# Kernel optimization log

Hardware: AMD Instinct MI355X
Metric: run time of the kernel (lower is better)

The kernel has to match this reference:

```python
import jax, jax.numpy as jnp
import numpy as np

N, D, E, L = 50000, 128, 800000, 3
BN_EPS = 1e-5


def _bn(h, mean, var, gamma, beta):
    # eval-mode BatchNorm1d with running statistics
    return (h - mean) * jax.lax.rsqrt(var + BN_EPS) * gamma + beta


def setup_inputs() -> dict:
    key = jax.random.key(0)
    ks = jax.random.split(key, 16)
    x = jax.random.normal(ks[0], (N, D), dtype=jnp.float32)
    edge_index = jax.random.randint(ks[1], (2, E), 0, N, dtype=jnp.int32)
    s = 1.0 / np.sqrt(D)
    W1 = jax.random.uniform(ks[2], (L, D, 2 * D), jnp.float32, -s, s)
    b1 = jax.random.uniform(ks[3], (L, 2 * D), jnp.float32, -s, s)
    g1 = jnp.ones((L, 2 * D), jnp.float32)
    be1 = jnp.zeros((L, 2 * D), jnp.float32)
    m1 = jax.random.normal(ks[4], (L, 2 * D), jnp.float32) * 0.1
    v1 = jax.random.uniform(ks[5], (L, 2 * D), jnp.float32, 0.5, 1.5)
    s2 = 1.0 / np.sqrt(2 * D)
    W2 = jax.random.uniform(ks[6], (L, 2 * D, D), jnp.float32, -s2, s2)
    b2 = jax.random.uniform(ks[7], (L, D), jnp.float32, -s2, s2)
    eps = jnp.zeros((L,), jnp.float32)  # train_eps=True, init 0
    go = jnp.ones((L - 1, D), jnp.float32)
    bo = jnp.zeros((L - 1, D), jnp.float32)
    mo = jax.random.normal(ks[8], (L - 1, D), jnp.float32) * 0.1
    vo = jax.random.uniform(ks[9], (L - 1, D), jnp.float32, 0.5, 1.5)
    return {"x": x, "edge_index": edge_index, "W1": W1, "b1": b1, "g1": g1,
            "be1": be1, "m1": m1, "v1": v1, "W2": W2, "b2": b2, "eps": eps,
            "go": go, "bo": bo, "mo": mo, "vo": vo}


def reference(x, edge_index, W1, b1, g1, be1, m1, v1, W2, b2, eps, go, bo, mo, vo):
    src, dst = edge_index[0], edge_index[1]
    n = x.shape[0]
    h = x
    for i in range(L):
        # GINConv: (1+eps)*x_i + sum_{j in N(i)} x_j, then MLP
        agg = jax.ops.segment_sum(h[src], dst, num_segments=n)  # [N, D]
        z = (1.0 + eps[i]) * h + agg
        z = jax.nn.relu(_bn(z @ W1[i] + b1[i], m1[i], v1[i], g1[i], be1[i]))
        z = z @ W2[i] + b2[i]
        if i < L - 1:
            z = jax.nn.relu(_bn(z, mo[i], vo[i], go[i], bo[i]))
            # dropout: identity in eval mode
        h = z
    return jax.nn.log_softmax(h, axis=-1)
```

## Files before the change

### kernel.cpp

```cpp
#include <hip/hip_runtime.h>
#include <hip/hip_bf16.h>

#define N_NODES 50000
#define DIM 128
#define E_EDGES 800000
#define L_LAYERS 3
#define MTILES 3125
#define MTPAD 3128
#define NBUCK 98
#define BCAP 9216
#define BSHIFT 9

typedef __attribute__((ext_vector_type(8))) short short8;
typedef __attribute__((ext_vector_type(4))) float f32x4;
typedef __attribute__((ext_vector_type(2))) _Float16 f16x2;
typedef __attribute__((ext_vector_type(4))) _Float16 f16x4;
typedef __attribute__((ext_vector_type(8))) _Float16 f16x8;

__global__ __launch_bounds__(256) void cvt16_kernel(const float4* __restrict__ in,
                                                    f16x4* __restrict__ out) {
    int i = blockIdx.x * 256 + threadIdx.x;
    float4 v = in[i];
    f16x4 o;
    o[0] = (_Float16)v.x; o[1] = (_Float16)v.y;
    o[2] = (_Float16)v.z; o[3] = (_Float16)v.w;
    out[i] = o;
}

__global__ __launch_bounds__(256) void trans_f16_kernel(
        const float* __restrict__ w1, const float* __restrict__ w2,
        _Float16* __restrict__ f1, _Float16* __restrict__ f2) {
    int idx = blockIdx.x * 256 + threadIdx.x;
    const int per = DIM * 2 * DIM;
    const int tot = L_LAYERS * per;
    const float* w;
    _Float16* f;
    int K, Nn, id;
    if (idx < tot) { w = w1; f = f1; K = DIM; Nn = 2 * DIM; id = idx; }
    else           { w = w2; f = f2; K = 2 * DIM; Nn = DIM; id = idx - tot; }
    int l = id / per;
    int r = id - l * per;
    int k = r / Nn;
    int n = r - k * Nn;
    int KS = K >> 5;
    int off = ((((n >> 4) * KS + (k >> 5)) * 4 + ((k >> 3) & 3)) * 16 + (n & 15)) * 8 + (k & 7);
    f[(size_t)l * per + off] = (_Float16)w[id];
}

__global__ __launch_bounds__(256) void prep_params_kernel(
        const float* __restrict__ b1, const float* __restrict__ g1,
        const float* __restrict__ be1, const float* __restrict__ m1,
        const float* __restrict__ v1, const float* __restrict__ b2,
        const float* __restrict__ go, const float* __restrict__ bo,
        const float* __restrict__ mo, const float* __restrict__ vo,
        float* __restrict__ scale1, float* __restrict__ shift1,
        float* __restrict__ scale2, float* __restrict__ shift2) {
    int idx = blockIdx.x * 256 + threadIdx.x;
    if (idx < L_LAYERS * 256) {
        float s = g1[idx] * rsqrtf(v1[idx] + 1e-5f);
        scale1[idx] = s;
        shift1[idx] = (b1[idx] - m1[idx]) * s + be1[idx];
    }
    int idx2 = idx - L_LAYERS * 256;
    if (idx2 >= 0 && idx2 < L_LAYERS * 128) {
        int l = idx2 >> 7;
        if (l < L_LAYERS - 1) {
            float s = go[idx2] * rsqrtf(vo[idx2] + 1e-5f);
            scale2[idx2] = s;
            shift2[idx2] = (b2[idx2] - mo[idx2]) * s + bo[idx2];
        } else {
            scale2[idx2] = 1.0f;
            shift2[idx2] = b2[idx2];
        }
    }
}


__global__ void initcur_kernel(int* __restrict__ gcur) {
    int t = threadIdx.x;
    if (t < NBUCK) gcur[t] = t * BCAP;
}

__global__ __launch_bounds__(256) void bin_kernel(const int* __restrict__ ei,
                                                  int* __restrict__ gcur,
                                                  unsigned int* __restrict__ brec) {
    __shared__ int cnt[NBUCK];
    __shared__ int off[NBUCK];
    __shared__ int gbase[NBUCK];
    __shared__ unsigned int rec[4096];
    const int t = threadIdx.x;
    const int start = blockIdx.x * 4096;
    for (int i = t; i < NBUCK; i += 256) cnt[i] = 0;
    __syncthreads();
    unsigned int myrec[16];
    unsigned int mypos[16];
    int nmine = 0;
    #pragma unroll
    for (int i = 0; i < 16; ++i) {
        int e = start + i * 256 + t;
        if (e < E_EDGES) {
            int src = ei[e];
            int dst = ei[E_EDGES + e];
            int b = dst >> BSHIFT;
            int idx = atomicAdd(&cnt[b], 1);
            myrec[i] = ((unsigned int)(dst & 511) << 16) | (unsigned int)src;
            mypos[i] = ((unsigned int)b << 16) | (unsigned int)idx;
            nmine = i + 1;
        }
    }
    __syncthreads();
    if (t == 0) {
        int s = 0;
        for (int b = 0; b < NBUCK; ++b) { off[b] = s; s += cnt[b]; }
    }
    __syncthreads();
    #pragma unroll
    for (int i = 0; i < 16; ++i) {
        if (i < nmine) {
            int b = mypos[i] >> 16;
            int idx = mypos[i] & 0xFFFF;
            rec[off[b] + idx] = myrec[i];
        }
    }
    __syncthreads();
    if (t < NBUCK && cnt[t] > 0) gbase[t] = atomicAdd(&gcur[t], cnt[t]);
    __syncthreads();
    const int wv = t >> 6, lane = t & 63;
    for (int b = wv; b < NBUCK; b += 4) {
        int c = cnt[b], o = off[b], g = gbase[b];
        for (int j = lane; j < c; j += 64)
            brec[g + j] = rec[o + j];
    }
}

__global__ void bscan_kernel(const int* __restrict__ gcur, int* __restrict__ colbase,
                             int* __restrict__ rowp) {
    if (threadIdx.x == 0) {
        int s = 0;
        for (int b = 0; b < NBUCK; ++b) {
            colbase[b] = s;
            s += gcur[b] - b * BCAP;
        }
        rowp[N_NODES] = E_EDGES;
    }
}

__global__ __launch_bounds__(256) void bsort_kernel(const unsigned int* __restrict__ brec,
                                                    const int* __restrict__ gcur,
                                                    const int* __restrict__ colbase,
                                                    int* __restrict__ rowp,
                                                    unsigned short* __restrict__ col) {
    __shared__ int ncnt[512];
    __shared__ int noff[512];
    __shared__ int wsum[4];
    __shared__ unsigned short srcbuf[BCAP];
    const int b = blockIdx.x;
    const int t = threadIdx.x;
    const int lane = t & 63;
    const int wv = t >> 6;
    const int cnt = gcur[b] - b * BCAP;
    const unsigned int* r = brec + (size_t)b * BCAP;
    for (int i = t; i < 512; i += 256) ncnt[i] = 0;
    __syncthreads();
    for (int j = t; j < cnt; j += 256)
        atomicAdd(&ncnt[r[j] >> 16], 1);
    __syncthreads();
    int a0 = ncnt[2 * t], a1 = ncnt[2 * t + 1];
    int pair = a0 + a1;
    int inc = pair;
    #pragma unroll
    for (int d = 1; d < 64; d <<= 1) {
        int u = __shfl_up(inc, d, 64);
        if (lane >= d) inc += u;
    }
    if (lane == 63) wsum[wv] = inc;
    __syncthreads();
    int wo = 0;
    if (wv > 0) wo = wsum[0];
    if (wv > 1) wo += wsum[1];
    if (wv > 2) wo += wsum[2];
    int excl = wo + inc - pair;
    noff[2 * t] = excl;
    noff[2 * t + 1] = excl + a0;
    __syncthreads();
    const int n0 = b << BSHIFT;
    const int cb = colbase[b];
    for (int i = t; i < 512; i += 256) {
        int node = n0 + i;
        if (node < N_NODES) rowp[node] = cb + noff[i];
    }
    for (int i = t; i < 512; i += 256) ncnt[i] = noff[i];
    __syncthreads();
    for (int j = t; j < cnt; j += 256) {
        unsigned int v = r[j];
        int pos = atomicAdd(&ncnt[v >> 16], 1);
        srcbuf[pos] = (unsigned short)(v & 0xFFFFu);
    }
    __syncthreads();
    unsigned short* cp = col + cb;
    for (int j = t; j < cnt; j += 256) cp[j] = srcbuf[j];
}

__global__ __launch_bounds__(256) void aggregate_kernel(
        const unsigned int* __restrict__ h16,
        const int* __restrict__ row, const unsigned short* __restrict__ col,
        const float* __restrict__ epsp,
        unsigned short* __restrict__ zf) {
    int wv = threadIdx.x >> 6;
    int lane = threadIdx.x & 63;
    int node = blockIdx.x * 4 + wv;
    size_t base = (size_t)node * 64;
    float s = 1.0f + epsp[0];
    f16x2 hv = __builtin_bit_cast(f16x2, h16[base + lane]);
    float ax = s * (float)hv[0], ay = s * (float)hv[1];
    int e = row[node], e1 = row[node + 1];
    for (; e + 8 <= e1; e += 8) {
        int c0 = col[e],     c1 = col[e + 1], c2 = col[e + 2], c3 = col[e + 3];
        int c4 = col[e + 4], c5 = col[e + 5], c6 = col[e + 6], c7 = col[e + 7];
        f16x2 v0 = __builtin_bit_cast(f16x2, h16[(size_t)c0 * 64 + lane]);
        f16x2 v1 = __builtin_bit_cast(f16x2, h16[(size_t)c1 * 64 + lane]);
        f16x2 v2 = __builtin_bit_cast(f16x2, h16[(size_t)c2 * 64 + lane]);
        f16x2 v3 = __builtin_bit_cast(f16x2, h16[(size_t)c3 * 64 + lane]);
        f16x2 v4 = __builtin_bit_cast(f16x2, h16[(size_t)c4 * 64 + lane]);
        f16x2 v5 = __builtin_bit_cast(f16x2, h16[(size_t)c5 * 64 + lane]);
        f16x2 v6 = __builtin_bit_cast(f16x2, h16[(size_t)c6 * 64 + lane]);
        f16x2 v7 = __builtin_bit_cast(f16x2, h16[(size_t)c7 * 64 + lane]);
        ax += (((float)v0[0] + (float)v1[0]) + ((float)v2[0] + (float)v3[0]))
            + (((float)v4[0] + (float)v5[0]) + ((float)v6[0] + (float)v7[0]));
        ay += (((float)v0[1] + (float)v1[1]) + ((float)v2[1] + (float)v3[1]))
            + (((float)v4[1] + (float)v5[1]) + ((float)v6[1] + (float)v7[1]));
    }
    for (; e < e1; ++e) {
        f16x2 v = __builtin_bit_cast(f16x2, h16[(size_t)col[e] * 64 + lane]);
        ax += (float)v[0];
        ay += (float)v[1];
    }
    unsigned short ux = __builtin_bit_cast(unsigned short, (_Float16)ax);
    unsigned short uy = __builtin_bit_cast(unsigned short, (_Float16)ay);
    int mt = node >> 4, r16 = node & 15;
    int ks = lane >> 4, quad = (lane >> 2) & 3, jb = (lane * 2) & 7;
    size_t zo = (((size_t)(mt * 4 + ks)) * 4 + quad) * 128 + r16 * 8 + jb;
    *(ushort2*)(zf + zo) = make_ushort2(ux, uy);
}

__global__ __launch_bounds__(256) void mlp_kernel(
        const _Float16* __restrict__ zf,
        const _Float16* __restrict__ w1f, const _Float16* __restrict__ w2f,
        const float* __restrict__ scale1, const float* __restrict__ shift1,
        const float* __restrict__ scale2, const float* __restrict__ shift2,
        int last,
        unsigned short* __restrict__ h16out, float* __restrict__ lsout) {
    __shared__ _Float16 wbuf[16384];
    __shared__ _Float16 tbuf[4][2176];
    const int tid = threadIdx.x;
    const int wave = tid >> 6;
    const int lane = tid & 63;
    const int quad = lane >> 4;
    const int l16 = lane & 15;
    const int mt = blockIdx.x * 4 + wave;
    const int R0 = mt * 16;

    f16x8 ah[4];
    #pragma unroll
    for (int ks = 0; ks < 4; ++ks)
        ah[ks] = *(const f16x8*)(zf + (((size_t)(mt * 4 + ks)) << 9) + lane * 8);

    f32x4 acc2[8] = {};
    #pragma unroll
    for (int c = 0; c < 2; ++c) {
        {
            const _Float16* g = w1f + c * 16384 + tid * 8;
            _Float16* l = wbuf + tid * 8;
            #pragma unroll
            for (int j = 0; j < 8; ++j)
                *(f16x8*)(l + j * 2048) = *(const f16x8*)(g + j * 2048);
        }
        __syncthreads();
        #pragma unroll
        for (int ntl = 0; ntl < 8; ++ntl) {
            f32x4 acc = {};
            #pragma unroll
            for (int ks = 0; ks < 4; ++ks) {
                f16x8 b = *(const f16x8*)&wbuf[(ntl * 4 + ks) * 512 + lane * 8];
                acc = __builtin_amdgcn_mfma_f32_16x16x32_f16(ah[ks], b, acc, 0, 0, 0);
            }
            int cg = (c * 8 + ntl) * 16 + l16;
            float sc = scale1[cg];
            float sh = shift1[cg];
            int plane = (cg >> 3) & 15;
            int basei = plane * 136 + (cg & 7);
            #pragma unroll
            for (int r = 0; r < 4; ++r) {
                float val = fmaxf(acc[r] * sc + sh, 0.0f);
                tbuf[wave][basei + (quad * 4 + r) * 8] = (_Float16)val;
            }
        }
        __syncthreads();
        {
            #pragma unroll
            for (int nt = 0; nt < 8; ++nt) {
                *(f16x8*)&wbuf[nt * 2048 + tid * 8] =
                    *(const f16x8*)(w2f + (((size_t)(nt * 8 + c * 4)) << 9) + tid * 8);
            }
        }
        __syncthreads();
        #pragma unroll
        for (int ks4 = 0; ks4 < 4; ++ks4) {
            int po = (ks4 * 4 + quad) * 136 + l16 * 8;
            f16x8 a2 = *(const f16x8*)&tbuf[wave][po];
            #pragma unroll
            for (int nt = 0; nt < 8; ++nt) {
                f16x8 b = *(const f16x8*)&wbuf[(nt * 4 + ks4) * 512 + lane * 8];
                acc2[nt] = __builtin_amdgcn_mfma_f32_16x16x32_f16(a2, b, acc2[nt], 0, 0, 0);
            }
        }
        __syncthreads();
    }

    #pragma unroll
    for (int nt = 0; nt < 8; ++nt) {
        int cg = nt * 16 + l16;
        float sc = scale2[cg];
        float sh = shift2[cg];
        #pragma unroll
        for (int r = 0; r < 4; ++r)
            acc2[nt][r] = acc2[nt][r] * sc + sh;
    }
    if (!last) {
        #pragma unroll
        for (int nt = 0; nt < 8; ++nt) {
            int cg = nt * 16 + l16;
            #pragma unroll
            for (int r = 0; r < 4; ++r) {
                int rg = R0 + quad * 4 + r;
                if (rg < N_NODES) {
                    float val = fmaxf(acc2[nt][r], 0.0f);
                    h16out[(size_t)rg * DIM + cg] =
                        __builtin_bit_cast(unsigned short, (_Float16)val);
                }
            }
        }
    } else {
        #pragma unroll
        for (int r = 0; r < 4; ++r) {
            float mx = acc2[0][r];
            #pragma unroll
            for (int nt = 1; nt < 8; ++nt) mx = fmaxf(mx, acc2[nt][r]);
            #pragma unroll
            for (int off = 1; off < 16; off <<= 1) mx = fmaxf(mx, __shfl_xor(mx, off, 64));
            float sum = 0.0f;
            #pragma unroll
            for (int nt = 0; nt < 8; ++nt) sum += expf(acc2[nt][r] - mx);
            #pragma unroll
            for (int off = 1; off < 16; off <<= 1) sum += __shfl_xor(sum, off, 64);
            float ls = mx + logf(sum);
            int rg = R0 + quad * 4 + r;
            if (rg < N_NODES) {
                #pragma unroll
                for (int nt = 0; nt < 8; ++nt)
                    lsout[(size_t)rg * DIM + nt * 16 + l16] = acc2[nt][r] - ls;
            }
        }
    }
}

extern "C" void kernel_launch(void* const* d_in, const int* in_sizes, int n_in,
                              void* d_out, int out_size, void* d_ws, size_t ws_size,
                              hipStream_t stream) {
    const float* x   = (const float*)d_in[0];
    const int*   ei  = (const int*)d_in[1];
    const float* W1  = (const float*)d_in[2];
    const float* b1  = (const float*)d_in[3];
    const float* g1  = (const float*)d_in[4];
    const float* be1 = (const float*)d_in[5];
    const float* m1  = (const float*)d_in[6];
    const float* v1  = (const float*)d_in[7];
    const float* W2  = (const float*)d_in[8];
    const float* b2  = (const float*)d_in[9];
    const float* eps = (const float*)d_in[10];
    const float* go  = (const float*)d_in[11];
    const float* bo  = (const float*)d_in[12];
    const float* mo  = (const float*)d_in[13];
    const float* vo  = (const float*)d_in[14];

    char* ws = (char*)d_ws;
    unsigned short* h16 = (unsigned short*)ws;  ws += (size_t)N_NODES * DIM * 2;
    unsigned short* zf = (unsigned short*)ws;   ws += (size_t)MTPAD * 2048 * 2;
    _Float16* w1f = (_Float16*)ws;              ws += (size_t)L_LAYERS * 32768 * 2;
    _Float16* w2f = (_Float16*)ws;              ws += (size_t)L_LAYERS * 32768 * 2;
    float* scale1 = (float*)ws; ws += (size_t)L_LAYERS * 256 * 4;
    float* shift1 = (float*)ws; ws += (size_t)L_LAYERS * 256 * 4;
    float* scale2 = (float*)ws; ws += (size_t)L_LAYERS * 128 * 4;
    float* shift2 = (float*)ws; ws += (size_t)L_LAYERS * 128 * 4;
    unsigned int* brec = (unsigned int*)ws; ws += (size_t)NBUCK * BCAP * 4;
    int* gcur    = (int*)ws; ws += 128 * 4;
    int* colbase = (int*)ws; ws += 128 * 4;
    int* rowp    = (int*)ws; ws += (size_t)(N_NODES + 1) * 4;
    unsigned short* col = (unsigned short*)ws; ws += (size_t)E_EDGES * 2;

    initcur_kernel<<<1, 128, 0, stream>>>(gcur);
    bin_kernel<<<(E_EDGES + 4095) / 4096, 256, 0, stream>>>(ei, gcur, brec);
    bscan_kernel<<<1, 64, 0, stream>>>(gcur, colbase, rowp);
    bsort_kernel<<<NBUCK, 256, 0, stream>>>(brec, gcur, colbase, rowp, col);

    cvt16_kernel<<<(N_NODES * DIM / 4) / 256, 256, 0, stream>>>((const float4*)x, (f16x4*)h16);
    trans_f16_kernel<<<(2 * L_LAYERS * DIM * 2 * DIM) / 256, 256, 0, stream>>>(W1, W2, w1f, w2f);
    prep_params_kernel<<<5, 256, 0, stream>>>(b1, g1, be1, m1, v1, b2, go, bo, mo, vo,
                                              scale1, shift1, scale2, shift2);

    for (int i = 0; i < L_LAYERS; ++i) {
        aggregate_kernel<<<N_NODES / 4, 256, 0, stream>>>((const unsigned int*)h16,
                                                          rowp, col, eps + i, zf);
        int last = (i == L_LAYERS - 1) ? 1 : 0;
        mlp_kernel<<<782, 256, 0, stream>>>((const _Float16*)zf,
            w1f + (size_t)i * 32768, w2f + (size_t)i * 32768,
            scale1 + i * 256, shift1 + i * 256,
            scale2 + i * 128, shift2 + i * 128,
            last, h16, (float*)d_out);
    }
}
```

Baseline: 326.8 us.

## Fuse neighbor aggregation into MLP kernel and merge setup launches

Each MLP wave now aggregates its own 16 nodes' neighbor features straight into shared memory, so the separate aggregate kernel and its zf round trip through global memory go away. Node features ping-pong between two fp16 buffers because a layer's output can no longer overwrite its input. The fp16 conversion, weight transpose, BN parameter prep and bucket counter init are merged into one setup launch, and the bucket prefix scan moves into bsort. This saves launches and global traffic, but aggregation parallelism drops from one wave per node to one wave per 16 nodes (782 blocks), which may hide gather latency less well.

```diff
diff --git a/kernel.cpp b/kernel.cpp
--- a/kernel.cpp
+++ b/kernel.cpp
@@ -1,85 +1,84 @@
 #include <hip/hip_runtime.h>
-#include <hip/hip_bf16.h>
 
 #define N_NODES 50000
 #define DIM 128
 #define E_EDGES 800000
 #define L_LAYERS 3
-#define MTILES 3125
 #define MTPAD 3128
 #define NBUCK 98
 #define BCAP 9216
 #define BSHIFT 9
 
-typedef __attribute__((ext_vector_type(8))) short short8;
+#define CVT_BLOCKS 6250
+#define TRANS_BLOCKS 768
+#define PREP_BLOCKS 5
+
 typedef __attribute__((ext_vector_type(4))) float f32x4;
 typedef __attribute__((ext_vector_type(2))) _Float16 f16x2;
 typedef __attribute__((ext_vector_type(4))) _Float16 f16x4;
 typedef __attribute__((ext_vector_type(8))) _Float16 f16x8;
 
-__global__ __launch_bounds__(256) void cvt16_kernel(const float4* __restrict__ in,
-                                                    f16x4* __restrict__ out) {
-    int i = blockIdx.x * 256 + threadIdx.x;
-    float4 v = in[i];
-    f16x4 o;
-    o[0] = (_Float16)v.x; o[1] = (_Float16)v.y;
-    o[2] = (_Float16)v.z; o[3] = (_Float16)v.w;
-    out[i] = o;
-}
-
-__global__ __launch_bounds__(256) void trans_f16_kernel(
+__global__ __launch_bounds__(256) void setup_kernel(
+        const float4* __restrict__ x4, f16x4* __restrict__ h16o,
         const float* __restrict__ w1, const float* __restrict__ w2,
-        _Float16* __restrict__ f1, _Float16* __restrict__ f2) {
-    int idx = blockIdx.x * 256 + threadIdx.x;
-    const int per = DIM * 2 * DIM;
-    const int tot = L_LAYERS * per;
-    const float* w;
-    _Float16* f;
-    int K, Nn, id;
-    if (idx < tot) { w = w1; f = f1; K = DIM; Nn = 2 * DIM; id = idx; }
-    else           { w = w2; f = f2; K = 2 * DIM; Nn = DIM; id = idx - tot; }
-    int l = id / per;
-    int r = id - l * per;
-    int k = r / Nn;
-    int n = r - k * Nn;
-    int KS = K >> 5;
-    int off = ((((n >> 4) * KS + (k >> 5)) * 4 + ((k >> 3) & 3)) * 16 + (n & 15)) * 8 + (k & 7);
-    f[(size_t)l * per + off] = (_Float16)w[id];
-}
-
-__global__ __launch_bounds__(256) void prep_params_kernel(
+        _Float16* __restrict__ f1, _Float16* __restrict__ f2,
         const float* __restrict__ b1, const float* __restrict__ g1,
         const float* __restrict__ be1, const float* __restrict__ m1,
         const float* __restrict__ v1, const float* __restrict__ b2,
         const float* __restrict__ go, const float* __restrict__ bo,
         const float* __restrict__ mo, const float* __restrict__ vo,
         float* __restrict__ scale1, float* __restrict__ shift1,
-        float* __restrict__ scale2, float* __restrict__ shift2) {
-    int idx = blockIdx.x * 256 + threadIdx.x;
-    if (idx < L_LAYERS * 256) {
-        float s = g1[idx] * rsqrtf(v1[idx] + 1e-5f);
-        scale1[idx] = s;
-        shift1[idx] = (b1[idx] - m1[idx]) * s + be1[idx];
-    }
-    int idx2 = idx - L_LAYERS * 256;
-    if (idx2 >= 0 && idx2 < L_LAYERS * 128) {
-        int l = idx2 >> 7;
-        if (l < L_LAYERS - 1) {
-            float s = go[idx2] * rsqrtf(vo[idx2] + 1e-5f);
-            scale2[idx2] = s;
-            shift2[idx2] = (b2[idx2] - mo[idx2]) * s + bo[idx2];
-        } else {
-            scale2[idx2] = 1.0f;
-            shift2[idx2] = b2[idx2];
-        }
+        float* __restrict__ scale2, float* __restrict__ shift2,
+        int* __restrict__ gcur) {
+    const int b = blockIdx.x;
+    const int t = threadIdx.x;
+    if (b < CVT_BLOCKS) {
+        int i = b * 256 + t;
+        float4 v = x4[i];
+        f16x4 o;
+        o[0] = (_Float16)v.x; o[1] = (_Float16)v.y;
+        o[2] = (_Float16)v.z; o[3] = (_Float16)v.w;
+        h16o[i] = o;
+    } else if (b < CVT_BLOCKS + TRANS_BLOCKS) {
+        int idx = (b - CVT_BLOCKS) * 256 + t;
+        const int per = DIM * 2 * DIM;
+        const int tot = L_LAYERS * per;
+        const float* w;
+        _Float16* f;
+        int K, Nn, id;
+        if (idx < tot) { w = w1; f = f1; K = DIM; Nn = 2 * DIM; id = idx; }
+        else           { w = w2; f = f2; K = 2 * DIM; Nn = DIM; id = idx - tot; }
+        int l = id / per;
+        int r = id - l * per;
+        int k = r / Nn;
+        int n = r - k * Nn;
+        int KS = K >> 5;
+        int off = ((((n >> 4) * KS + (k >> 5)) * 4 + ((k >> 3) & 3)) * 16 + (n & 15)) * 8 + (k & 7);
+        f[(size_t)l * per + off] = (_Float16)w[id];
+    } else if (b < CVT_BLOCKS + TRANS_BLOCKS + PREP_BLOCKS) {
+        int idx = (b - (CVT_BLOCKS + TRANS_BLOCKS)) * 256 + t;
+        if (idx < L_LAYERS * 256) {
+            float sv = g1[idx] * rsqrtf(v1[idx] + 1e-5f);
+            scale1[idx] = sv;
+            shift1[idx] = (b1[idx] - m1[idx]) * sv + be1[idx];
+        }
+        int idx2 = idx - L_LAYERS * 256;
+        if (idx2 >= 0 && idx2 < L_LAYERS * 128) {
+            int l = idx2 >> 7;
+            if (l < L_LAYERS - 1) {
+                float sv = go[idx2] * rsqrtf(vo[idx2] + 1e-5f);
+                scale2[idx2] = sv;
+                shift2[idx2] = (b2[idx2] - mo[idx2]) * sv + bo[idx2];
+            } else {
+                scale2[idx2] = 1.0f;
+                shift2[idx2] = b2[idx2];
+            }
+        }
+    } else {
+        if (t < NBUCK) gcur[t] = t * BCAP;
     }
 }
 
-
-__global__ void initcur_kernel(int* __restrict__ gcur) {
-    int t = threadIdx.x;
-    if (t < NBUCK) gcur[t] = t * BCAP;
-}
 
 __global__ __launch_bounds__(256) void bin_kernel(const int* __restrict__ ei,
                                                   int* __restrict__ gcur,
@@ -133,21 +132,8 @@
     }
 }
 
-__global__ void bscan_kernel(const int* __restrict__ gcur, int* __restrict__ colbase,
-                             int* __restrict__ rowp) {
-    if (threadIdx.x == 0) {
-        int s = 0;
-        for (int b = 0; b < NBUCK; ++b) {
-            colbase[b] = s;
-            s += gcur[b] - b * BCAP;
-        }
-        rowp[N_NODES] = E_EDGES;
-    }
-}
-
 __global__ __launch_bounds__(256) void bsort_kernel(const unsigned int* __restrict__ brec,
                                                     const int* __restrict__ gcur,
-                                                    const int* __restrict__ colbase,
                                                     int* __restrict__ rowp,
                                                     unsigned short* __restrict__ col) {
     __shared__ int ncnt[512];
@@ -158,10 +144,16 @@
     const int t = threadIdx.x;
     const int lane = t & 63;
     const int wv = t >> 6;
+    int pv = (t < b) ? (gcur[t] - t * BCAP) : 0;
+    #pragma unroll
+    for (int d = 1; d < 64; d <<= 1) pv += __shfl_xor(pv, d, 64);
+    if (lane == 0) wsum[wv] = pv;
+    if (b == 0 && t == 0) rowp[N_NODES] = E_EDGES;
     const int cnt = gcur[b] - b * BCAP;
     const unsigned int* r = brec + (size_t)b * BCAP;
     for (int i = t; i < 512; i += 256) ncnt[i] = 0;
     __syncthreads();
+    const int cb = wsum[0] + wsum[1] + wsum[2] + wsum[3];
     for (int j = t; j < cnt; j += 256)
         atomicAdd(&ncnt[r[j] >> 16], 1);
     __syncthreads();
@@ -184,7 +176,6 @@
     noff[2 * t + 1] = excl + a0;
     __syncthreads();
     const int n0 = b << BSHIFT;
-    const int cb = colbase[b];
     for (int i = t; i < 512; i += 256) {
         int node = n0 + i;
         if (node < N_NODES) rowp[node] = cb + noff[i];
@@ -201,50 +192,10 @@
     for (int j = t; j < cnt; j += 256) cp[j] = srcbuf[j];
 }
 
-__global__ __launch_bounds__(256) void aggregate_kernel(
+__global__ __launch_bounds__(256) void fused_kernel(
         const unsigned int* __restrict__ h16,
         const int* __restrict__ row, const unsigned short* __restrict__ col,
         const float* __restrict__ epsp,
-        unsigned short* __restrict__ zf) {
-    int wv = threadIdx.x >> 6;
-    int lane = threadIdx.x & 63;
-    int node = blockIdx.x * 4 + wv;
-    size_t base = (size_t)node * 64;
-    float s = 1.0f + epsp[0];
-    f16x2 hv = __builtin_bit_cast(f16x2, h16[base + lane]);
-    float ax = s * (float)hv[0], ay = s * (float)hv[1];
-    int e = row[node], e1 = row[node + 1];
-    for (; e + 8 <= e1; e += 8) {
-        int c0 = col[e],     c1 = col[e + 1], c2 = col[e + 2], c3 = col[e + 3];
-        int c4 = col[e + 4], c5 = col[e + 5], c6 = col[e + 6], c7 = col[e + 7];
-        f16x2 v0 = __builtin_bit_cast(f16x2, h16[(size_t)c0 * 64 + lane]);
-        f16x2 v1 = __builtin_bit_cast(f16x2, h16[(size_t)c1 * 64 + lane]);
-        f16x2 v2 = __builtin_bit_cast(f16x2, h16[(size_t)c2 * 64 + lane]);
-        f16x2 v3 = __builtin_bit_cast(f16x2, h16[(size_t)c3 * 64 + lane]);
-        f16x2 v4 = __builtin_bit_cast(f16x2, h16[(size_t)c4 * 64 + lane]);
-        f16x2 v5 = __builtin_bit_cast(f16x2, h16[(size_t)c5 * 64 + lane]);
-        f16x2 v6 = __builtin_bit_cast(f16x2, h16[(size_t)c6 * 64 + lane]);
-        f16x2 v7 = __builtin_bit_cast(f16x2, h16[(size_t)c7 * 64 + lane]);
-        ax += (((float)v0[0] + (float)v1[0]) + ((float)v2[0] + (float)v3[0]))
-            + (((float)v4[0] + (float)v5[0]) + ((float)v6[0] + (float)v7[0]));
-        ay += (((float)v0[1] + (float)v1[1]) + ((float)v2[1] + (float)v3[1]))
-            + (((float)v4[1] + (float)v5[1]) + ((float)v6[1] + (float)v7[1]));
-    }
-    for (; e < e1; ++e) {
-        f16x2 v = __builtin_bit_cast(f16x2, h16[(size_t)col[e] * 64 + lane]);
-        ax += (float)v[0];
-        ay += (float)v[1];
-    }
-    unsigned short ux = __builtin_bit_cast(unsigned short, (_Float16)ax);
-    unsigned short uy = __builtin_bit_cast(unsigned short, (_Float16)ay);
-    int mt = node >> 4, r16 = node & 15;
-    int ks = lane >> 4, quad = (lane >> 2) & 3, jb = (lane * 2) & 7;
-    size_t zo = (((size_t)(mt * 4 + ks)) * 4 + quad) * 128 + r16 * 8 + jb;
-    *(ushort2*)(zf + zo) = make_ushort2(ux, uy);
-}
-
-__global__ __launch_bounds__(256) void mlp_kernel(
-        const _Float16* __restrict__ zf,
         const _Float16* __restrict__ w1f, const _Float16* __restrict__ w2f,
         const float* __restrict__ scale1, const float* __restrict__ shift1,
         const float* __restrict__ scale2, const float* __restrict__ shift2,
@@ -260,10 +211,49 @@
     const int mt = blockIdx.x * 4 + wave;
     const int R0 = mt * 16;
 
+    {
+        const float s = 1.0f + epsp[0];
+        for (int i = 0; i < 16; ++i) {
+            const int node = R0 + i;
+            float ax = 0.0f, ay = 0.0f;
+            if (node < N_NODES) {
+                f16x2 hv = __builtin_bit_cast(f16x2, h16[(size_t)node * 64 + lane]);
+                ax = s * (float)hv[0];
+                ay = s * (float)hv[1];
+                int e = row[node], e1 = row[node + 1];
+                for (; e + 8 <= e1; e += 8) {
+                    int c0 = col[e],     c1 = col[e + 1], c2 = col[e + 2], c3 = col[e + 3];
+                    int c4 = col[e + 4], c5 = col[e + 5], c6 = col[e + 6], c7 = col[e + 7];
+                    f16x2 v0 = __builtin_bit_cast(f16x2, h16[(size_t)c0 * 64 + lane]);
+                    f16x2 v1 = __builtin_bit_cast(f16x2, h16[(size_t)c1 * 64 + lane]);
+                    f16x2 v2 = __builtin_bit_cast(f16x2, h16[(size_t)c2 * 64 + lane]);
+                    f16x2 v3 = __builtin_bit_cast(f16x2, h16[(size_t)c3 * 64 + lane]);
+                    f16x2 v4 = __builtin_bit_cast(f16x2, h16[(size_t)c4 * 64 + lane]);
+                    f16x2 v5 = __builtin_bit_cast(f16x2, h16[(size_t)c5 * 64 + lane]);
+                    f16x2 v6 = __builtin_bit_cast(f16x2, h16[(size_t)c6 * 64 + lane]);
+                    f16x2 v7 = __builtin_bit_cast(f16x2, h16[(size_t)c7 * 64 + lane]);
+                    ax += (((float)v0[0] + (float)v1[0]) + ((float)v2[0] + (float)v3[0]))
+                        + (((float)v4[0] + (float)v5[0]) + ((float)v6[0] + (float)v7[0]));
+                    ay += (((float)v0[1] + (float)v1[1]) + ((float)v2[1] + (float)v3[1]))
+                        + (((float)v4[1] + (float)v5[1]) + ((float)v6[1] + (float)v7[1]));
+                }
+                for (; e < e1; ++e) {
+                    f16x2 v = __builtin_bit_cast(f16x2, h16[(size_t)col[e] * 64 + lane]);
+                    ax += (float)v[0];
+                    ay += (float)v[1];
+                }
+            }
+            f16x2 p;
+            p[0] = (_Float16)ax;
+            p[1] = (_Float16)ay;
+            *(f16x2*)&tbuf[wave][i * 136 + lane * 2] = p;
+        }
+    }
+
     f16x8 ah[4];
     #pragma unroll
     for (int ks = 0; ks < 4; ++ks)
-        ah[ks] = *(const f16x8*)(zf + (((size_t)(mt * 4 + ks)) << 9) + lane * 8);
+        ah[ks] = *(const f16x8*)&tbuf[wave][l16 * 136 + ks * 32 + quad * 8];
 
     f32x4 acc2[8] = {};
     #pragma unroll
@@ -281,8 +271,8 @@
             f32x4 acc = {};
             #pragma unroll
             for (int ks = 0; ks < 4; ++ks) {
-                f16x8 b = *(const f16x8*)&wbuf[(ntl * 4 + ks) * 512 + lane * 8];
-                acc = __builtin_amdgcn_mfma_f32_16x16x32_f16(ah[ks], b, acc, 0, 0, 0);
+                f16x8 bfr = *(const f16x8*)&wbuf[(ntl * 4 + ks) * 512 + lane * 8];
+                acc = __builtin_amdgcn_mfma_f32_16x16x32_f16(ah[ks], bfr, acc, 0, 0, 0);
             }
             int cg = (c * 8 + ntl) * 16 + l16;
             float sc = scale1[cg];
@@ -310,8 +300,8 @@
             f16x8 a2 = *(const f16x8*)&tbuf[wave][po];
             #pragma unroll
             for (int nt = 0; nt < 8; ++nt) {
-                f16x8 b = *(const f16x8*)&wbuf[(nt * 4 + ks4) * 512 + lane * 8];
-                acc2[nt] = __builtin_amdgcn_mfma_f32_16x16x32_f16(a2, b, acc2[nt], 0, 0, 0);
+                f16x8 bfr = *(const f16x8*)&wbuf[(nt * 4 + ks4) * 512 + lane * 8];
+                acc2[nt] = __builtin_amdgcn_mfma_f32_16x16x32_f16(a2, bfr, acc2[nt], 0, 0, 0);
             }
         }
         __syncthreads();
@@ -384,8 +374,8 @@
     const float* vo  = (const float*)d_in[14];
 
     char* ws = (char*)d_ws;
-    unsigned short* h16 = (unsigned short*)ws;  ws += (size_t)N_NODES * DIM * 2;
-    unsigned short* zf = (unsigned short*)ws;   ws += (size_t)MTPAD * 2048 * 2;
+    unsigned short* h16a = (unsigned short*)ws; ws += (size_t)N_NODES * DIM * 2;
+    unsigned short* h16b = (unsigned short*)ws; ws += (size_t)N_NODES * DIM * 2;
     _Float16* w1f = (_Float16*)ws;              ws += (size_t)L_LAYERS * 32768 * 2;
     _Float16* w2f = (_Float16*)ws;              ws += (size_t)L_LAYERS * 32768 * 2;
     float* scale1 = (float*)ws; ws += (size_t)L_LAYERS * 256 * 4;
@@ -393,29 +383,26 @@
     float* scale2 = (float*)ws; ws += (size_t)L_LAYERS * 128 * 4;
     float* shift2 = (float*)ws; ws += (size_t)L_LAYERS * 128 * 4;
     unsigned int* brec = (unsigned int*)ws; ws += (size_t)NBUCK * BCAP * 4;
-    int* gcur    = (int*)ws; ws += 128 * 4;
-    int* colbase = (int*)ws; ws += 128 * 4;
-    int* rowp    = (int*)ws; ws += (size_t)(N_NODES + 1) * 4;
+    int* gcur = (int*)ws; ws += 128 * 4;
+    int* rowp = (int*)ws; ws += (size_t)(N_NODES + 1) * 4;
     unsigned short* col = (unsigned short*)ws; ws += (size_t)E_EDGES * 2;
 
-    initcur_kernel<<<1, 128, 0, stream>>>(gcur);
+    setup_kernel<<<CVT_BLOCKS + TRANS_BLOCKS + PREP_BLOCKS + 1, 256, 0, stream>>>(
+        (const float4*)x, (f16x4*)h16a, W1, W2, w1f, w2f,
+        b1, g1, be1, m1, v1, b2, go, bo, mo, vo,
+        scale1, shift1, scale2, shift2, gcur);
     bin_kernel<<<(E_EDGES + 4095) / 4096, 256, 0, stream>>>(ei, gcur, brec);
-    bscan_kernel<<<1, 64, 0, stream>>>(gcur, colbase, rowp);
-    bsort_kernel<<<NBUCK, 256, 0, stream>>>(brec, gcur, colbase, rowp, col);
-
-    cvt16_kernel<<<(N_NODES * DIM / 4) / 256, 256, 0, stream>>>((const float4*)x, (f16x4*)h16);
-    trans_f16_kernel<<<(2 * L_LAYERS * DIM * 2 * DIM) / 256, 256, 0, stream>>>(W1, W2, w1f, w2f);
-    prep_params_kernel<<<5, 256, 0, stream>>>(b1, g1, be1, m1, v1, b2, go, bo, mo, vo,
-                                              scale1, shift1, scale2, shift2);
+    bsort_kernel<<<NBUCK, 256, 0, stream>>>(brec, gcur, rowp, col);
 
     for (int i = 0; i < L_LAYERS; ++i) {
-        aggregate_kernel<<<N_NODES / 4, 256, 0, stream>>>((const unsigned int*)h16,
-                                                          rowp, col, eps + i, zf);
+        const unsigned short* hin = (i & 1) ? h16b : h16a;
+        unsigned short* hout = (i & 1) ? h16a : h16b;
         int last = (i == L_LAYERS - 1) ? 1 : 0;
-        mlp_kernel<<<782, 256, 0, stream>>>((const _Float16*)zf,
+        fused_kernel<<<MTPAD / 4, 256, 0, stream>>>(
+            (const unsigned int*)hin, rowp, col, eps + i,
             w1f + (size_t)i * 32768, w2f + (size_t)i * 32768,
             scale1 + i * 256, shift1 + i * 256,
             scale2 + i * 128, shift2 + i * 128,
-            last, h16, (float*)d_out);
+            last, hout, (float*)d_out);
     }
 }
```

New measurement: 502.3 us. 1.54x slower.
